# Performance work log

Hardware: AMD Instinct MI355X
Metric: run time of the kernel (lower is better)

## Reference

```python
import jax, jax.numpy as jnp
import numpy as np
from jax.ops import segment_sum, segment_max

N, F_IN, HID, HEADS, NCLS, E = 50000, 256, 64, 8, 16, 400000
NEG_SLOPE = 0.2


def setup_inputs() -> dict:
    key = jax.random.key(0)
    ks = jax.random.split(key, 10)
    x = jax.random.normal(ks[0], (N, F_IN), dtype=jnp.float32)
    edge_index = jax.random.randint(ks[1], (2, E), 0, N, dtype=jnp.int64)
    s1 = 1.0 / np.sqrt(F_IN)
    s2 = 1.0 / np.sqrt(HID * HEADS)
    return {
        "x": x,
        "edge_index": edge_index,
        "W1": jax.random.normal(ks[2], (F_IN, HEADS * HID), dtype=jnp.float32) * s1,
        "a_src1": jax.random.normal(ks[3], (HEADS, HID), dtype=jnp.float32) * 0.1,
        "a_dst1": jax.random.normal(ks[4], (HEADS, HID), dtype=jnp.float32) * 0.1,
        "b1": jnp.zeros((HEADS * HID,), dtype=jnp.float32),
        "W2": jax.random.normal(ks[5], (HEADS * HID, NCLS), dtype=jnp.float32) * s2,
        "a_src2": jax.random.normal(ks[6], (1, NCLS), dtype=jnp.float32) * 0.1,
        "a_dst2": jax.random.normal(ks[7], (1, NCLS), dtype=jnp.float32) * 0.1,
        "b2": jnp.zeros((NCLS,), dtype=jnp.float32),
    }


def _gat_conv(x, src, dst, W, a_src, a_dst, bias, heads, out_c, concat):
    n = x.shape[0]
    h = (x @ W).reshape(n, heads, out_c)          # [N, H, C]
    # per-node attention halves (PyG trick: dot before gather)
    al_src = jnp.einsum('nhc,hc->nh', h, a_src)    # [N, H]
    al_dst = jnp.einsum('nhc,hc->nh', h, a_dst)    # [N, H]
    alpha = al_src[src] + al_dst[dst]              # [E, H]
    alpha = jax.nn.leaky_relu(alpha, NEG_SLOPE)
    # segment softmax over destination neighborhoods
    m = segment_max(alpha, dst, num_segments=n)
    ex = jnp.exp(alpha - m[dst])
    denom = segment_sum(ex, dst, num_segments=n)
    alpha = ex / denom[dst]                        # [E, H]
    msg = h[src] * alpha[:, :, None]               # [E, H, C]
    out = segment_sum(msg, dst, num_segments=n)    # [N, H, C]
    if concat:
        out = out.reshape(n, heads * out_c)
    else:
        out = out.mean(axis=1)
    return out + bias


def reference(x, edge_index, W1, a_src1, a_dst1, b1, W2, a_src2, a_dst2, b2):
    n = x.shape[0]
    # PyG GATConv default: add self-loops
    loop = jnp.arange(n, dtype=edge_index.dtype)
    src = jnp.concatenate([edge_index[0], loop])
    dst = jnp.concatenate([edge_index[1], loop])
    h = _gat_conv(x, src, dst, W1, a_src1, a_dst1, b1, HEADS, HID, True)
    h = jax.nn.elu(h)
    # dropout layers are identity in eval mode
    out = _gat_conv(h, src, dst, W2, a_src2, a_dst2, b2, 1, NCLS, False)
    return out
```

## Files before the change

### kernel.cpp

```cpp
#include <hip/hip_runtime.h>
#include <hip/hip_bf16.h>
#include <math.h>

#define N_NODES 50000
#define F_INK   256
#define HEADS   8
#define HID     64
#define HH      512
#define NCLS    16
#define NEDGE   400000
#define NEG_SLOPE 0.2f

#define BCOLS 64
#define KPAD  264
#define NBLK_SCAN ((N_NODES + 255) / 256)

typedef __attribute__((ext_vector_type(8))) short short8;
typedef __attribute__((ext_vector_type(4))) short sh4;
typedef __attribute__((ext_vector_type(4))) float float4v;

__device__ __forceinline__ float bf2f(unsigned short u){
    unsigned int x = ((unsigned int)u) << 16;
    float f; __builtin_memcpy(&f, &x, 4); return f;
}
__device__ __forceinline__ unsigned short f2bf(float f){
    unsigned int x; __builtin_memcpy(&x, &f, 4);
    unsigned int r = x + 0x7FFFu + ((x >> 16) & 1u);
    return (unsigned short)(r >> 16);
}
__device__ __forceinline__ float lrelu(float a){ return a > 0.f ? a : NEG_SLOPE * a; }

__device__ __forceinline__ void fma8(float* acc, float w, short8 v){
    unsigned int u[4]; __builtin_memcpy(u, &v, 16);
#pragma unroll
    for (int j = 0; j < 4; j++){
        acc[2*j]   += w * __uint_as_float(u[j] << 16);
        acc[2*j+1] += w * __uint_as_float(u[j] & 0xffff0000u);
    }
}

__global__ void cvt_f32_bf16(const float* __restrict__ in, unsigned short* __restrict__ out, int n4){
    int i = blockIdx.x * blockDim.x + threadIdx.x;
    int stride = gridDim.x * blockDim.x;
    for (; i < n4; i += stride){
        float4v f = *(const float4v*)(in + (size_t)i * 4);
        sh4 o;
#pragma unroll
        for (int j = 0; j < 4; j++) o[j] = (short)f2bf(f[j]);
        *(sh4*)(out + (size_t)i * 4) = o;
    }
}

__global__ void cvt_weights(const float* __restrict__ W1, unsigned short* __restrict__ W1T,
                            const float* __restrict__ W2, unsigned short* __restrict__ W2T){
    int i = blockIdx.x * blockDim.x + threadIdx.x;
    if (i < F_INK * HH){
        int k = i / HH, c = i % HH;
        W1T[c * F_INK + k] = f2bf(W1[i]);
    }
    int j = i - F_INK * HH;
    if (j >= 0 && j < HH * NCLS){
        int k = j / NCLS, c = j % NCLS;
        W2T[c * HH + k] = f2bf(W2[j]);
    }
}

__global__ void count_edges(const int* __restrict__ dst, int* __restrict__ counts,
                            int* __restrict__ erank){
    int e = blockIdx.x * blockDim.x + threadIdx.x;
    if (e < NEDGE) erank[e] = atomicAdd(&counts[dst[e]], 1);
}

__global__ __launch_bounds__(256) void scan_part(const int* __restrict__ counts,
                                                 int* __restrict__ blocksums){
    __shared__ int red[256];
    int i = blockIdx.x * 256 + threadIdx.x;
    int v = (i < N_NODES) ? counts[i] : 0;
    red[threadIdx.x] = v; __syncthreads();
    for (int off = 128; off > 0; off >>= 1){
        if (threadIdx.x < off) red[threadIdx.x] += red[threadIdx.x + off];
        __syncthreads();
    }
    if (threadIdx.x == 0) blocksums[blockIdx.x] = red[0];
}

__global__ __launch_bounds__(256) void scan_top(const int* __restrict__ blocksums,
                                                int* __restrict__ blockbase,
                                                int* __restrict__ offsets){
    __shared__ int s[256];
    int t = threadIdx.x;
    int v = (t < NBLK_SCAN) ? blocksums[t] : 0;
    s[t] = v; __syncthreads();
    int val = v;
    for (int off = 1; off < 256; off <<= 1){
        int o2 = (t >= off) ? s[t - off] : 0;
        __syncthreads();
        val += o2; s[t] = val;
        __syncthreads();
    }
    if (t < NBLK_SCAN) blockbase[t] = val - v;
    if (t == 255) offsets[N_NODES] = s[255];
}

__global__ __launch_bounds__(256) void scan_write(const int* __restrict__ counts,
                                                  const int* __restrict__ blockbase,
                                                  int* __restrict__ offsets){
    __shared__ int s[256];
    int i = blockIdx.x * 256 + threadIdx.x;
    int t = threadIdx.x;
    int v = (i < N_NODES) ? counts[i] : 0;
    s[t] = v; __syncthreads();
    int val = v;
    for (int off = 1; off < 256; off <<= 1){
        int o2 = (t >= off) ? s[t - off] : 0;
        __syncthreads();
        val += o2; s[t] = val;
        __syncthreads();
    }
    if (i < N_NODES) offsets[i] = blockbase[blockIdx.x] + val - v;
}

__global__ void scatter_edges(const int* __restrict__ src, const int* __restrict__ dst,
                              const int* __restrict__ offsets, const int* __restrict__ erank,
                              int* __restrict__ esrc){
    int e = blockIdx.x * blockDim.x + threadIdx.x;
    if (e < NEDGE) esrc[offsets[dst[e]] + erank[e]] = src[e];
}

__global__ __launch_bounds__(256) void gemm1(const unsigned short* __restrict__ xb,
                                             const unsigned short* __restrict__ w1t,
                                             const float* __restrict__ a_src,
                                             const float* __restrict__ a_dst,
                                             unsigned short* __restrict__ h1b,
                                             float* __restrict__ al_s,
                                             float* __restrict__ al_d){
    __shared__ unsigned short bs[BCOLS * KPAD];
    int cb  = blockIdx.x & 7;
    int rg  = blockIdx.x >> 3;
    int nrg = gridDim.x >> 3;
    {
        int kc = threadIdx.x & 31;
        int c0 = threadIdx.x >> 5;
#pragma unroll
        for (int it = 0; it < 8; it++){
            int col = it * 8 + c0;
            short8 v = *(const short8*)(w1t + (size_t)(cb * BCOLS + col) * F_INK + kc * 8);
            *(short8*)(&bs[col * KPAD + kc * 8]) = v;
        }
    }
    __syncthreads();
    int w    = threadIdx.x >> 6;
    int lane = threadIdx.x & 63;
    int lr = lane & 15, lk = lane >> 4;
    float a_s[4], a_d[4];
#pragma unroll
    for (int ct = 0; ct < 4; ct++){
        a_s[ct] = a_src[cb * HID + ct * 16 + lr];
        a_d[ct] = a_dst[cb * HID + ct * 16 + lr];
    }
    const int nchunk = (N_NODES + 127) / 128;
    for (int ch = rg; ch < nchunk; ch += nrg){
        int rb0 = ch * 128 + w * 32;
        if (rb0 >= N_NODES) continue;
        bool t1 = (rb0 + 16 < N_NODES);
        short8 a0[8], a1[8];
#pragma unroll
        for (int ks = 0; ks < 8; ks++)
            a0[ks] = *(const short8*)(xb + (size_t)(rb0 + lr) * F_INK + ks * 32 + lk * 8);
        if (t1){
#pragma unroll
            for (int ks = 0; ks < 8; ks++)
                a1[ks] = *(const short8*)(xb + (size_t)(rb0 + 16 + lr) * F_INK + ks * 32 + lk * 8);
        }
        float ds0[4] = {0.f,0.f,0.f,0.f}, dd0[4] = {0.f,0.f,0.f,0.f};
        float ds1[4] = {0.f,0.f,0.f,0.f}, dd1[4] = {0.f,0.f,0.f,0.f};
#pragma unroll
        for (int ct = 0; ct < 4; ct++){
            float4v acc0 = {0.f, 0.f, 0.f, 0.f};
            float4v acc1 = {0.f, 0.f, 0.f, 0.f};
#pragma unroll
            for (int ks = 0; ks < 8; ks++){
                short8 b = *(const short8*)(&bs[(ct * 16 + lr) * KPAD + ks * 32 + lk * 8]);
                acc0 = __builtin_amdgcn_mfma_f32_16x16x32_bf16(a0[ks], b, acc0, 0, 0, 0);
                if (t1) acc1 = __builtin_amdgcn_mfma_f32_16x16x32_bf16(a1[ks], b, acc1, 0, 0, 0);
            }
#pragma unroll
            for (int r = 0; r < 4; r++){
                h1b[(size_t)(rb0 + lk * 4 + r) * HH + cb * BCOLS + ct * 16 + lr] = f2bf(acc0[r]);
                ds0[r] += acc0[r] * a_s[ct];
                dd0[r] += acc0[r] * a_d[ct];
            }
            if (t1){
#pragma unroll
                for (int r = 0; r < 4; r++){
                    h1b[(size_t)(rb0 + 16 + lk * 4 + r) * HH + cb * BCOLS + ct * 16 + lr] = f2bf(acc1[r]);
                    ds1[r] += acc1[r] * a_s[ct];
                    dd1[r] += acc1[r] * a_d[ct];
                }
            }
        }
#pragma unroll
        for (int r = 0; r < 4; r++){
#pragma unroll
            for (int o = 1; o < 16; o <<= 1){
                ds0[r] += __shfl_xor(ds0[r], o);
                dd0[r] += __shfl_xor(dd0[r], o);
                ds1[r] += __shfl_xor(ds1[r], o);
                dd1[r] += __shfl_xor(dd1[r], o);
            }
        }
        if (lr == 0){
#pragma unroll
            for (int r = 0; r < 4; r++){
                al_s[(rb0 + lk * 4 + r) * HEADS + cb] = ds0[r];
                al_d[(rb0 + lk * 4 + r) * HEADS + cb] = dd0[r];
            }
            if (t1){
#pragma unroll
                for (int r = 0; r < 4; r++){
                    al_s[(rb0 + 16 + lk * 4 + r) * HEADS + cb] = ds1[r];
                    al_d[(rb0 + 16 + lk * 4 + r) * HEADS + cb] = dd1[r];
                }
            }
        }
    }
}

__global__ __launch_bounds__(256) void softmax1(
        const float* __restrict__ al_s, const float* __restrict__ al_d,
        const int* __restrict__ offsets, const int* __restrict__ esrc,
        float* __restrict__ ew, float* __restrict__ wselfr, float* __restrict__ dinv){
    int d = blockIdx.x * 4 + (threadIdx.x >> 6);
    int lane = threadIdx.x & 63;
    if (d >= N_NODES) return;
    int h = lane & 7, i = lane >> 3;
    int off = offsets[d], deg = offsets[d + 1] - off;
    float ald = al_d[d * HEADS + h];
    float aself = lrelu(al_s[d * HEADS + h] + ald);
    float m = aself;
    for (int base = 0; base < deg; base += 8){
        int e = base + i;
        float a = -1e30f;
        if (e < deg) a = lrelu(al_s[esrc[off + e] * HEADS + h] + ald);
        a = fmaxf(a, __shfl_xor(a, 8));
        a = fmaxf(a, __shfl_xor(a, 16));
        a = fmaxf(a, __shfl_xor(a, 32));
        m = fmaxf(m, a);
    }
    float denom = __expf(aself - m);
    for (int base = 0; base < deg; base += 8){
        int e = base + i;
        float w = 0.f;
        if (e < deg){
            w = __expf(lrelu(al_s[esrc[off + e] * HEADS + h] + ald) - m);
            ew[(size_t)(off + e) * HEADS + h] = w;
        }
        float ws = w;
        ws += __shfl_xor(ws, 8);
        ws += __shfl_xor(ws, 16);
        ws += __shfl_xor(ws, 32);
        denom += ws;
    }
    if (i == 0){
        wselfr[d * HEADS + h] = __expf(aself - m);
        dinv[d * HEADS + h]   = 1.f / denom;
    }
}

__global__ __launch_bounds__(256) void agg1(const unsigned short* __restrict__ h1b,
        const float* __restrict__ ew, const float* __restrict__ wselfr,
        const float* __restrict__ dinv,
        const int* __restrict__ offsets, const int* __restrict__ esrc,
        const float* __restrict__ b1, unsigned short* __restrict__ x2b){
    int d = blockIdx.x * 4 + (threadIdx.x >> 6);
    if (d >= N_NODES) return;
    int lane = threadIdx.x & 63;
    int g = lane >> 3;
    int cb = g * HID + (lane & 7) * 8;
    int off = offsets[d], deg = offsets[d + 1] - off;
    float acc[8];
    {
        float w0 = wselfr[d * HEADS + g];
        short8 v = *(const short8*)(h1b + (size_t)d * HH + cb);
        unsigned int u[4]; __builtin_memcpy(u, &v, 16);
#pragma unroll
        for (int j = 0; j < 4; j++){
            acc[2*j]   = w0 * __uint_as_float(u[j] << 16);
            acc[2*j+1] = w0 * __uint_as_float(u[j] & 0xffff0000u);
        }
    }
    int e = 0;
    for (; e + 4 <= deg; e += 4){
        int s0 = __builtin_amdgcn_readfirstlane(esrc[off + e]);
        int s1 = __builtin_amdgcn_readfirstlane(esrc[off + e + 1]);
        int s2 = __builtin_amdgcn_readfirstlane(esrc[off + e + 2]);
        int s3 = __builtin_amdgcn_readfirstlane(esrc[off + e + 3]);
        float w0 = ew[(size_t)(off + e)     * HEADS + g];
        float w1 = ew[(size_t)(off + e + 1) * HEADS + g];
        float w2 = ew[(size_t)(off + e + 2) * HEADS + g];
        float w3 = ew[(size_t)(off + e + 3) * HEADS + g];
        short8 v0 = *(const short8*)(h1b + (size_t)s0 * HH + cb);
        short8 v1 = *(const short8*)(h1b + (size_t)s1 * HH + cb);
        short8 v2 = *(const short8*)(h1b + (size_t)s2 * HH + cb);
        short8 v3 = *(const short8*)(h1b + (size_t)s3 * HH + cb);
        fma8(acc, w0, v0); fma8(acc, w1, v1);
        fma8(acc, w2, v2); fma8(acc, w3, v3);
    }
    for (; e < deg; e++){
        int s0 = __builtin_amdgcn_readfirstlane(esrc[off + e]);
        float w0 = ew[(size_t)(off + e) * HEADS + g];
        short8 v0 = *(const short8*)(h1b + (size_t)s0 * HH + cb);
        fma8(acc, w0, v0);
    }
    float di = dinv[d * HEADS + g];
    unsigned short o8[8];
#pragma unroll
    for (int j = 0; j < 8; j++){
        float v = acc[j] * di + b1[cb + j];
        v = v > 0.f ? v : __expf(v) - 1.f;
        o8[j] = f2bf(v);
    }
    short8 ov; __builtin_memcpy(&ov, o8, 16);
    *(short8*)(x2b + (size_t)d * HH + cb) = ov;
}

__global__ __launch_bounds__(256) void gemm2(const unsigned short* __restrict__ x2b,
        const unsigned short* __restrict__ w2t,
        const float* __restrict__ a_s2, const float* __restrict__ a_d2,
        float* __restrict__ h2, float* __restrict__ al2s, float* __restrict__ al2d){
    int wave = (blockIdx.x * blockDim.x + threadIdx.x) >> 6;
    int lane = threadIdx.x & 63;
    if (wave >= N_NODES / 16) return;
    int rowbase = wave * 16;
    int lr = lane & 15, lk = lane >> 4;
    float4v acc = {0.f, 0.f, 0.f, 0.f};
#pragma unroll
    for (int ks = 0; ks < 16; ks++){
        short8 a = *(const short8*)(x2b + (size_t)(rowbase + lr) * HH + ks * 32 + lk * 8);
        short8 b = *(const short8*)(w2t + (size_t)lr * HH + ks * 32 + lk * 8);
        acc = __builtin_amdgcn_mfma_f32_16x16x32_bf16(a, b, acc, 0, 0, 0);
    }
#pragma unroll
    for (int r = 0; r < 4; r++)
        h2[(size_t)(rowbase + lk * 4 + r) * NCLS + lr] = acc[r];
    float s_a = a_s2[lr], d_a = a_d2[lr];
#pragma unroll
    for (int r = 0; r < 4; r++){
        float ps = acc[r] * s_a, pd = acc[r] * d_a;
#pragma unroll
        for (int off = 1; off < 16; off <<= 1){
            ps += __shfl_xor(ps, off);
            pd += __shfl_xor(pd, off);
        }
        if (lr == 0){
            al2s[rowbase + lk * 4 + r] = ps;
            al2d[rowbase + lk * 4 + r] = pd;
        }
    }
}

__global__ __launch_bounds__(256) void agg2(const float* __restrict__ h2,
        const float* __restrict__ al2s, const float* __restrict__ al2d,
        const int* __restrict__ offsets, const int* __restrict__ esrc,
        const float* __restrict__ b2, float* __restrict__ out){
    int d = blockIdx.x * 4 + (threadIdx.x >> 6);
    int lane = threadIdx.x & 63;
    if (d >= N_NODES) return;
    int off = offsets[d], deg = offsets[d + 1] - off;
    float ald = al2d[d];
    float a0 = lrelu(al2s[d] + ald);
    float m = a0;
    for (int base = 0; base < deg; base += 64){
        int e = base + lane;
        float a = (e < deg) ? lrelu(al2s[esrc[off + e]] + ald) : -1e30f;
#pragma unroll
        for (int o = 1; o < 64; o <<= 1) a = fmaxf(a, __shfl_xor(a, o));
        m = fmaxf(m, a);
    }
    float dsum = __expf(a0 - m);
    for (int base = 0; base < deg; base += 64){
        int e = base + lane;
        float w = (e < deg) ? __expf(lrelu(al2s[esrc[off + e]] + ald) - m) : 0.f;
#pragma unroll
        for (int o = 1; o < 64; o <<= 1) w += __shfl_xor(w, o);
        dsum += w;
    }
    int sg = lane >> 4, col = lane & 15;
    float acc = (sg == 0) ? __expf(a0 - m) * h2[(size_t)d * NCLS + col] : 0.f;
    for (int i = sg; i < deg; i += 4){
        int s = esrc[off + i];
        float w = __expf(lrelu(al2s[s] + ald) - m);
        acc += w * h2[(size_t)s * NCLS + col];
    }
    acc += __shfl_xor(acc, 16);
    acc += __shfl_xor(acc, 32);
    if (lane < NCLS) out[(size_t)d * NCLS + lane] = acc / dsum + b2[lane];
}

extern "C" void kernel_launch(void* const* d_in, const int* in_sizes, int n_in,
                              void* d_out, int out_size, void* d_ws, size_t ws_size,
                              hipStream_t stream){
    const float* x   = (const float*)d_in[0];
    const int*   ei  = (const int*)d_in[1];
    const int*   src = ei;
    const int*   dst = ei + NEDGE;
    const float* W1  = (const float*)d_in[2];
    const float* as1 = (const float*)d_in[3];
    const float* ad1 = (const float*)d_in[4];
    const float* b1  = (const float*)d_in[5];
    const float* W2  = (const float*)d_in[6];
    const float* as2 = (const float*)d_in[7];
    const float* ad2 = (const float*)d_in[8];
    const float* b2  = (const float*)d_in[9];
    float* out = (float*)d_out;

    char* p = (char*)d_ws;
    auto carve = [&](size_t bytes) -> char* {
        char* r = p; p += (bytes + 255) & ~(size_t)255; return r;
    };
    unsigned short* xb   = (unsigned short*)carve((size_t)N_NODES * F_INK * 2);
    unsigned short* w1t  = (unsigned short*)carve((size_t)HH * F_INK * 2);
    unsigned short* w2t  = (unsigned short*)carve((size_t)HH * NCLS * 2);
    unsigned short* h1b  = (unsigned short*)carve((size_t)N_NODES * HH * 2);
    float* al1s  = (float*)carve((size_t)N_NODES * HEADS * 4);
    float* al1d  = (float*)carve((size_t)N_NODES * HEADS * 4);
    int* counts  = (int*)carve((size_t)N_NODES * 4);
    int* erank   = (int*)carve((size_t)NEDGE * 4);
    int* offsets = (int*)carve((size_t)(N_NODES + 1) * 4);
    int* blocksums = (int*)carve((size_t)NBLK_SCAN * 4);
    int* blockbase = (int*)carve((size_t)NBLK_SCAN * 4);
    int* esrc    = (int*)carve((size_t)NEDGE * 4);
    float* ew    = (float*)carve((size_t)NEDGE * HEADS * 4);
    float* wselfr= (float*)carve((size_t)N_NODES * HEADS * 4);
    float* dinv  = (float*)carve((size_t)N_NODES * HEADS * 4);
    unsigned short* x2b = (unsigned short*)carve((size_t)N_NODES * HH * 2);
    float* h2    = (float*)carve((size_t)N_NODES * NCLS * 4);
    float* al2s  = (float*)carve((size_t)N_NODES * 4);
    float* al2d  = (float*)carve((size_t)N_NODES * 4);
    if ((size_t)(p - (char*)d_ws) > ws_size) return;

    hipMemsetAsync(counts, 0, N_NODES * 4, stream);

    cvt_f32_bf16<<<2048, 256, 0, stream>>>(x, xb, N_NODES * F_INK / 4);
    cvt_weights<<<(F_INK * HH + HH * NCLS + 255) / 256, 256, 0, stream>>>(W1, w1t, W2, w2t);
    count_edges<<<(NEDGE + 255) / 256, 256, 0, stream>>>(dst, counts, erank);
    scan_part<<<NBLK_SCAN, 256, 0, stream>>>(counts, blocksums);
    scan_top<<<1, 256, 0, stream>>>(blocksums, blockbase, offsets);
    scan_write<<<NBLK_SCAN, 256, 0, stream>>>(counts, blockbase, offsets);
    scatter_edges<<<(NEDGE + 255) / 256, 256, 0, stream>>>(src, dst, offsets, erank, esrc);
    gemm1<<<8 * 128, 256, 0, stream>>>(xb, w1t, as1, ad1, h1b, al1s, al1d);
    softmax1<<<(N_NODES + 3) / 4, 256, 0, stream>>>(al1s, al1d, offsets, esrc, ew, wselfr, dinv);
    agg1<<<(N_NODES + 3) / 4, 256, 0, stream>>>(h1b, ew, wselfr, dinv, offsets, esrc, b1, x2b);
    gemm2<<<(N_NODES / 16 + 3) / 4, 256, 0, stream>>>(x2b, w2t, as2, ad2, h2, al2s, al2d);
    agg2<<<(N_NODES + 3) / 4, 256, 0, stream>>>(h2, al2s, al2d, offsets, esrc, b2, out);
}
```

Measured before the change: 250.1 us.

## Fuse layer-1 aggregation with layer-2 GEMM through shared memory

Merges agg1 and gemm2 into one kernel. Each block aggregates 16 destination nodes, four per wave, and stages the ELU'd bf16 features in padded LDS. One wave then runs the MFMA projection to 16 classes plus the attention dot products. This drops the 50000x512 bf16 x2b round trip to global memory and one kernel launch. In exchange each wave now handles four nodes serially, giving less parallelism per node, and three of four waves sit idle during the GEMM phase.

```diff
diff --git a/kernel.cpp b/kernel.cpp
--- a/kernel.cpp
+++ b/kernel.cpp
@@ -14,6 +14,8 @@
 #define BCOLS 64
 #define KPAD  264
 #define NBLK_SCAN ((N_NODES + 255) / 256)
+#define X2ROW 584
+#define X2GB  72
 
 typedef __attribute__((ext_vector_type(8))) short short8;
 typedef __attribute__((ext_vector_type(4))) short sh4;
@@ -267,94 +269,98 @@
     }
 }
 
-__global__ __launch_bounds__(256) void agg1(const unsigned short* __restrict__ h1b,
+__global__ __launch_bounds__(256) void agg1f(const unsigned short* __restrict__ h1b,
         const float* __restrict__ ew, const float* __restrict__ wselfr,
         const float* __restrict__ dinv,
         const int* __restrict__ offsets, const int* __restrict__ esrc,
-        const float* __restrict__ b1, unsigned short* __restrict__ x2b){
-    int d = blockIdx.x * 4 + (threadIdx.x >> 6);
-    if (d >= N_NODES) return;
-    int lane = threadIdx.x & 63;
-    int g = lane >> 3;
-    int cb = g * HID + (lane & 7) * 8;
-    int off = offsets[d], deg = offsets[d + 1] - off;
-    float acc[8];
-    {
-        float w0 = wselfr[d * HEADS + g];
-        short8 v = *(const short8*)(h1b + (size_t)d * HH + cb);
-        unsigned int u[4]; __builtin_memcpy(u, &v, 16);
-#pragma unroll
-        for (int j = 0; j < 4; j++){
-            acc[2*j]   = w0 * __uint_as_float(u[j] << 16);
-            acc[2*j+1] = w0 * __uint_as_float(u[j] & 0xffff0000u);
-        }
-    }
-    int e = 0;
-    for (; e + 4 <= deg; e += 4){
-        int s0 = __builtin_amdgcn_readfirstlane(esrc[off + e]);
-        int s1 = __builtin_amdgcn_readfirstlane(esrc[off + e + 1]);
-        int s2 = __builtin_amdgcn_readfirstlane(esrc[off + e + 2]);
-        int s3 = __builtin_amdgcn_readfirstlane(esrc[off + e + 3]);
-        float w0 = ew[(size_t)(off + e)     * HEADS + g];
-        float w1 = ew[(size_t)(off + e + 1) * HEADS + g];
-        float w2 = ew[(size_t)(off + e + 2) * HEADS + g];
-        float w3 = ew[(size_t)(off + e + 3) * HEADS + g];
-        short8 v0 = *(const short8*)(h1b + (size_t)s0 * HH + cb);
-        short8 v1 = *(const short8*)(h1b + (size_t)s1 * HH + cb);
-        short8 v2 = *(const short8*)(h1b + (size_t)s2 * HH + cb);
-        short8 v3 = *(const short8*)(h1b + (size_t)s3 * HH + cb);
-        fma8(acc, w0, v0); fma8(acc, w1, v1);
-        fma8(acc, w2, v2); fma8(acc, w3, v3);
-    }
-    for (; e < deg; e++){
-        int s0 = __builtin_amdgcn_readfirstlane(esrc[off + e]);
-        float w0 = ew[(size_t)(off + e) * HEADS + g];
-        short8 v0 = *(const short8*)(h1b + (size_t)s0 * HH + cb);
-        fma8(acc, w0, v0);
-    }
-    float di = dinv[d * HEADS + g];
-    unsigned short o8[8];
-#pragma unroll
-    for (int j = 0; j < 8; j++){
-        float v = acc[j] * di + b1[cb + j];
-        v = v > 0.f ? v : __expf(v) - 1.f;
-        o8[j] = f2bf(v);
-    }
-    short8 ov; __builtin_memcpy(&ov, o8, 16);
-    *(short8*)(x2b + (size_t)d * HH + cb) = ov;
-}
-
-__global__ __launch_bounds__(256) void gemm2(const unsigned short* __restrict__ x2b,
+        const float* __restrict__ b1,
         const unsigned short* __restrict__ w2t,
         const float* __restrict__ a_s2, const float* __restrict__ a_d2,
         float* __restrict__ h2, float* __restrict__ al2s, float* __restrict__ al2d){
-    int wave = (blockIdx.x * blockDim.x + threadIdx.x) >> 6;
+    __shared__ unsigned short x2l[16 * X2ROW];
+    int w = threadIdx.x >> 6;
     int lane = threadIdx.x & 63;
-    if (wave >= N_NODES / 16) return;
-    int rowbase = wave * 16;
-    int lr = lane & 15, lk = lane >> 4;
-    float4v acc = {0.f, 0.f, 0.f, 0.f};
-#pragma unroll
-    for (int ks = 0; ks < 16; ks++){
-        short8 a = *(const short8*)(x2b + (size_t)(rowbase + lr) * HH + ks * 32 + lk * 8);
-        short8 b = *(const short8*)(w2t + (size_t)lr * HH + ks * 32 + lk * 8);
-        acc = __builtin_amdgcn_mfma_f32_16x16x32_bf16(a, b, acc, 0, 0, 0);
-    }
-#pragma unroll
-    for (int r = 0; r < 4; r++)
-        h2[(size_t)(rowbase + lk * 4 + r) * NCLS + lr] = acc[r];
-    float s_a = a_s2[lr], d_a = a_d2[lr];
-#pragma unroll
-    for (int r = 0; r < 4; r++){
-        float ps = acc[r] * s_a, pd = acc[r] * d_a;
-#pragma unroll
-        for (int off = 1; off < 16; off <<= 1){
-            ps += __shfl_xor(ps, off);
-            pd += __shfl_xor(pd, off);
-        }
-        if (lr == 0){
-            al2s[rowbase + lk * 4 + r] = ps;
-            al2d[rowbase + lk * 4 + r] = pd;
+    int g = lane >> 3, i = lane & 7;
+    int cb = g * HID + i * 8;
+#pragma unroll
+    for (int q = 0; q < 4; q++){
+        int row = w * 4 + q;
+        int d = blockIdx.x * 16 + row;
+        int off = offsets[d], deg = offsets[d + 1] - off;
+        float acc[8];
+        {
+            float w0 = wselfr[d * HEADS + g];
+            short8 v = *(const short8*)(h1b + (size_t)d * HH + cb);
+            unsigned int u[4]; __builtin_memcpy(u, &v, 16);
+#pragma unroll
+            for (int j = 0; j < 4; j++){
+                acc[2*j]   = w0 * __uint_as_float(u[j] << 16);
+                acc[2*j+1] = w0 * __uint_as_float(u[j] & 0xffff0000u);
+            }
+        }
+        int e = 0;
+        for (; e + 4 <= deg; e += 4){
+            int s0 = __builtin_amdgcn_readfirstlane(esrc[off + e]);
+            int s1 = __builtin_amdgcn_readfirstlane(esrc[off + e + 1]);
+            int s2 = __builtin_amdgcn_readfirstlane(esrc[off + e + 2]);
+            int s3 = __builtin_amdgcn_readfirstlane(esrc[off + e + 3]);
+            float w0 = ew[(size_t)(off + e)     * HEADS + g];
+            float w1 = ew[(size_t)(off + e + 1) * HEADS + g];
+            float w2 = ew[(size_t)(off + e + 2) * HEADS + g];
+            float w3 = ew[(size_t)(off + e + 3) * HEADS + g];
+            short8 v0 = *(const short8*)(h1b + (size_t)s0 * HH + cb);
+            short8 v1 = *(const short8*)(h1b + (size_t)s1 * HH + cb);
+            short8 v2 = *(const short8*)(h1b + (size_t)s2 * HH + cb);
+            short8 v3 = *(const short8*)(h1b + (size_t)s3 * HH + cb);
+            fma8(acc, w0, v0); fma8(acc, w1, v1);
+            fma8(acc, w2, v2); fma8(acc, w3, v3);
+        }
+        for (; e < deg; e++){
+            int s0 = __builtin_amdgcn_readfirstlane(esrc[off + e]);
+            float w0 = ew[(size_t)(off + e) * HEADS + g];
+            short8 v0 = *(const short8*)(h1b + (size_t)s0 * HH + cb);
+            fma8(acc, w0, v0);
+        }
+        float di = dinv[d * HEADS + g];
+        unsigned short o8[8];
+#pragma unroll
+        for (int j = 0; j < 8; j++){
+            float v = acc[j] * di + b1[cb + j];
+            v = v > 0.f ? v : __expf(v) - 1.f;
+            o8[j] = f2bf(v);
+        }
+        short8 ov; __builtin_memcpy(&ov, o8, 16);
+        *(short8*)(&x2l[row * X2ROW + g * X2GB + i * 8]) = ov;
+    }
+    __syncthreads();
+    if (w == 0){
+        int rowbase = blockIdx.x * 16;
+        int lr = lane & 15, lk = lane >> 4;
+        float4v accv = {0.f, 0.f, 0.f, 0.f};
+#pragma unroll
+        for (int ks = 0; ks < 16; ks++){
+            int c0 = ks * 32 + lk * 8;
+            int gg = c0 >> 6, wc = c0 & 63;
+            short8 a = *(const short8*)(&x2l[lr * X2ROW + gg * X2GB + wc]);
+            short8 b = *(const short8*)(w2t + (size_t)lr * HH + ks * 32 + lk * 8);
+            accv = __builtin_amdgcn_mfma_f32_16x16x32_bf16(a, b, accv, 0, 0, 0);
+        }
+#pragma unroll
+        for (int r = 0; r < 4; r++)
+            h2[(size_t)(rowbase + lk * 4 + r) * NCLS + lr] = accv[r];
+        float s_a = a_s2[lr], d_a = a_d2[lr];
+#pragma unroll
+        for (int r = 0; r < 4; r++){
+            float ps = accv[r] * s_a, pd = accv[r] * d_a;
+#pragma unroll
+            for (int off = 1; off < 16; off <<= 1){
+                ps += __shfl_xor(ps, off);
+                pd += __shfl_xor(pd, off);
+            }
+            if (lr == 0){
+                al2s[rowbase + lk * 4 + r] = ps;
+                al2d[rowbase + lk * 4 + r] = pd;
+            }
         }
     }
 }
@@ -433,7 +439,6 @@
     float* ew    = (float*)carve((size_t)NEDGE * HEADS * 4);
     float* wselfr= (float*)carve((size_t)N_NODES * HEADS * 4);
     float* dinv  = (float*)carve((size_t)N_NODES * HEADS * 4);
-    unsigned short* x2b = (unsigned short*)carve((size_t)N_NODES * HH * 2);
     float* h2    = (float*)carve((size_t)N_NODES * NCLS * 4);
     float* al2s  = (float*)carve((size_t)N_NODES * 4);
     float* al2d  = (float*)carve((size_t)N_NODES * 4);
@@ -450,7 +455,7 @@
     scatter_edges<<<(NEDGE + 255) / 256, 256, 0, stream>>>(src, dst, offsets, erank, esrc);
     gemm1<<<8 * 128, 256, 0, stream>>>(xb, w1t, as1, ad1, h1b, al1s, al1d);
     softmax1<<<(N_NODES + 3) / 4, 256, 0, stream>>>(al1s, al1d, offsets, esrc, ew, wselfr, dinv);
-    agg1<<<(N_NODES + 3) / 4, 256, 0, stream>>>(h1b, ew, wselfr, dinv, offsets, esrc, b1, x2b);
-    gemm2<<<(N_NODES / 16 + 3) / 4, 256, 0, stream>>>(x2b, w2t, as2, ad2, h2, al2s, al2d);
+    agg1f<<<N_NODES / 16, 256, 0, stream>>>(h1b, ew, wselfr, dinv, offsets, esrc, b1,
+                                            w2t, as2, ad2, h2, al2s, al2d);
     agg2<<<(N_NODES + 3) / 4, 256, 0, stream>>>(h2, al2s, al2d, offsets, esrc, b2, out);
 }
```

Result: faster. 234.8 us (-6.1%).
